# Kernel tuning notes

Hardware: AMD Instinct MI355X
Metric: run time of the kernel (lower is better)

The kernel has to match this reference:

```python
import jax, jax.numpy as jnp
import numpy as np

N = 6144; E = 98304; H = 256; HEADS = 4; NE = 8; TOPK = 2; S = 400; L = 3; V = 1024; T = 768
GAMMA = 2.0; LAMBDA_SPD = 0.5


def _ln(x, g, b):
    m = x.mean(-1, keepdims=True)
    v = ((x - m) ** 2).mean(-1, keepdims=True)
    return (x - m) / jnp.sqrt(v + 1e-5) * g + b


def _gelu(x):
    return jax.nn.gelu(x, approximate=False)


def _cos(a, b):
    # torch F.cosine_similarity with eps=1e-8
    na = jnp.maximum(jnp.linalg.norm(a, axis=-1), 1e-8)
    nb = jnp.maximum(jnp.linalg.norm(b, axis=-1), 1e-8)
    return (a * b).sum(-1) / (na * nb)


def setup_inputs():
    key = jax.random.key(0)
    ks = jax.random.split(key, 30)
    w = lambda k, s: jax.random.normal(k, s, dtype=jnp.float32) * 0.02
    z = lambda s: jnp.zeros(s, jnp.float32)
    o = lambda s: jnp.ones(s, jnp.float32)
    return dict(
        feat_v=jax.random.normal(ks[0], (N, V), dtype=jnp.float32),
        feat_t=jax.random.normal(ks[1], (N, T), dtype=jnp.float32),
        spd_matrix=jax.random.uniform(ks[2], (N, N), dtype=jnp.float32) * 8.0,
        proj_v_w=w(ks[3], (V, H)), proj_v_b=z((H,)),
        proj_t_w=w(ks[4], (T, H)), proj_t_b=z((H,)),
        mask_token=jax.random.normal(ks[5], (H,), dtype=jnp.float32),
        gate_w=w(ks[6], (H, NE)), gate_b=z((NE,)),
        moe_w1=w(ks[7], (NE, H, H)), moe_b1=z((NE, H)),
        moe_ln_g=o((NE, H)), moe_ln_b=z((NE, H)),
        moe_w2=w(ks[8], (NE, H, H)), moe_b2=z((NE, H)),
        gat_fc=w(ks[9], (L, H, HEADS * H)),
        gat_al=w(ks[10], (L, HEADS, H)), gat_ar=w(ks[11], (L, HEADS, H)),
        gat_bias=z((L, HEADS, H)),
        dec_v_w1=w(ks[12], (H, H)), dec_v_b1=z((H,)),
        dec_v_ln_g=o((H,)), dec_v_ln_b=z((H,)),
        dec_v_w2=w(ks[13], (H, V)), dec_v_b2=z((V,)),
        dec_t_w1=w(ks[14], (H, H)), dec_t_b1=z((H,)),
        dec_t_ln_g=o((H,)), dec_t_ln_b=z((H,)),
        dec_t_w2=w(ks[15], (H, T)), dec_t_b2=z((T,)),
        spd_w1=w(ks[16], (2 * H, H)), spd_b1=z((H,)),
        spd_ln_g=o((H,)), spd_ln_b=z((H,)),
        spd_w2=w(ks[17], (H, 1)), spd_b2=z((1,)),
        src=jax.random.randint(ks[18], (E,), 0, N, dtype=jnp.int32),
        dst=jax.random.randint(ks[19], (E,), 0, N, dtype=jnp.int32),
        mask_int=jax.random.randint(ks[20], (N,), 0, 10, dtype=jnp.int32),
        sample_idx=jnp.sort(jax.random.randint(ks[21], (S,), 0, N, dtype=jnp.int32)),
    )


def _forward(feat_v, feat_t, spd_matrix, proj_v_w, proj_v_b, proj_t_w, proj_t_b, mask_token,
             gate_w, gate_b, moe_w1, moe_b1, moe_ln_g, moe_ln_b, moe_w2, moe_b2,
             gat_fc, gat_al, gat_ar, gat_bias,
             dec_v_w1, dec_v_b1, dec_v_ln_g, dec_v_ln_b, dec_v_w2, dec_v_b2,
             dec_t_w1, dec_t_b1, dec_t_ln_g, dec_t_ln_b, dec_t_w2, dec_t_b2,
             spd_w1, spd_b1, spd_ln_g, spd_ln_b, spd_w2, spd_b2,
             src, dst, mask_int, sample_idx):
    # project each domain to hidden and average (stack(...).mean(0))
    x = ((feat_v @ proj_v_w + proj_v_b) + (feat_t @ proj_t_w + proj_t_b)) * 0.5  # [N,H]
    mask = mask_int == 0  # ~feat_drop_rate of nodes
    x = jnp.where(mask[:, None], mask_token[None, :], x)
    # --- MoE: softmax gate, top-2 routing, dense experts ---
    gate = jax.nn.softmax(x @ gate_w + gate_b, axis=-1)          # [N,NE]
    tw, ti = jax.lax.top_k(gate, TOPK)
    tw = tw / tw.sum(-1, keepdims=True)
    eh = _gelu(_ln(jnp.einsum('nh,ehk->nek', x, moe_w1) + moe_b1, moe_ln_g, moe_ln_b))
    eo = jnp.einsum('nek,ekj->nej', eh, moe_w2) + moe_b2         # [N,NE,H]
    sel = jnp.take_along_axis(eo, ti[:, :, None], axis=1)        # [N,TOPK,H]
    h = (sel * tw[:, :, None]).sum(axis=1)                       # [N,H]
    # --- GATConv layers (dgl semantics), mean over heads ---
    for l in range(L):
        z = (h @ gat_fc[l]).reshape(N, HEADS, H)                 # [N,heads,H]
        el = (z * gat_al[l]).sum(-1)                             # [N,heads]
        er = (z * gat_ar[l]).sum(-1)
        e = jax.nn.leaky_relu(el[src] + er[dst], negative_slope=0.2)  # [E,heads]
        m = jax.ops.segment_max(e, dst, num_segments=N)
        ex = jnp.exp(e - m[dst])
        den = jax.ops.segment_sum(ex, dst, num_segments=N)
        alpha = ex / jnp.where(den > 0, den, 1.0)[dst]
        out = jax.ops.segment_sum(alpha[:, :, None] * z[src], dst, num_segments=N)
        h = (out + gat_bias[l]).mean(axis=1)                     # [N,H]
    # --- focal cosine reconstruction loss over masked nodes ---
    maskf = mask.astype(h.dtype)
    nm = jnp.maximum(maskf.sum(), 1.0)
    rec = jnp.zeros((), h.dtype)
    for w1, b1, g, b, w2, b2, tgt in ((dec_v_w1, dec_v_b1, dec_v_ln_g, dec_v_ln_b, dec_v_w2, dec_v_b2, feat_v),
                                      (dec_t_w1, dec_t_b1, dec_t_ln_g, dec_t_ln_b, dec_t_w2, dec_t_b2, feat_t)):
        r = _gelu(_ln(h @ w1 + b1, g, b)) @ w2 + b2
        sim = _cos(r, tgt)
        rec = rec + (((1.0 - sim) ** GAMMA) * maskf).sum() / nm
    # --- SPD loss on S sampled nodes, pairwise MLP decode ---
    se = h[sample_idx]                                           # [S,H]
    li = se @ spd_w1[:H]                                         # cat([xi,xj]) @ W1 split
    lj = se @ spd_w1[H:]
    pre = li[:, None, :] + lj[None, :, :] + spd_b1               # [S,S,H]
    pred = (_gelu(_ln(pre, spd_ln_g, spd_ln_b)) @ spd_w2)[..., 0] + spd_b2[0]
    strue = spd_matrix[sample_idx][:, sample_idx]
    spd_loss = jnp.mean((pred - strue) ** 2)
    total = rec + LAMBDA_SPD * spd_loss
    return total, h


def reference(feat_v, feat_t, spd_matrix, proj_v_w, proj_v_b, proj_t_w, proj_t_b, mask_token,
              gate_w, gate_b, moe_w1, moe_b1, moe_ln_g, moe_ln_b, moe_w2, moe_b2,
              gat_fc, gat_al, gat_ar, gat_bias,
              dec_v_w1, dec_v_b1, dec_v_ln_g, dec_v_ln_b, dec_v_w2, dec_v_b2,
              dec_t_w1, dec_t_b1, dec_t_ln_g, dec_t_ln_b, dec_t_w2, dec_t_b2,
              spd_w1, spd_b1, spd_ln_g, spd_ln_b, spd_w2, spd_b2,
              src, dst, mask_int, sample_idx):
    return _forward(feat_v, feat_t, spd_matrix, proj_v_w, proj_v_b, proj_t_w, proj_t_b, mask_token,
                    gate_w, gate_b, moe_w1, moe_b1, moe_ln_g, moe_ln_b, moe_w2, moe_b2,
                    gat_fc, gat_al, gat_ar, gat_bias,
                    dec_v_w1, dec_v_b1, dec_v_ln_g, dec_v_ln_b, dec_v_w2, dec_v_b2,
                    dec_t_w1, dec_t_b1, dec_t_ln_g, dec_t_ln_b, dec_t_w2, dec_t_b2,
                    spd_w1, spd_b1, spd_ln_g, spd_ln_b, spd_w2, spd_b2,
                    src, dst, mask_int, sample_idx)
```

## Files before the change

### kernel.cpp

```cpp
#include <hip/hip_runtime.h>

#define NN 6144
#define EE 98304
#define HH 256
#define NHEADS 4
#define NEXP 8
#define SS 400
#define VV 1024
#define TT 768

__device__ __forceinline__ float wave_allsum(float v){
  #pragma unroll
  for (int off=32; off; off>>=1) v += __shfl_xor(v, off, 64);
  return v;
}
__device__ __forceinline__ float wave_allmax(float v){
  #pragma unroll
  for (int off=32; off; off>>=1) v = fmaxf(v, __shfl_xor(v, off, 64));
  return v;
}
__device__ __forceinline__ float block_allsum(float v, float* red){
  int t = threadIdx.x;
  v = wave_allsum(v);
  __syncthreads();
  if ((t & 63) == 0) red[t >> 6] = v;
  __syncthreads();
  return red[0] + red[1] + red[2] + red[3];
}
__device__ __forceinline__ float gelu_exact(float x){
  return 0.5f * x * (1.0f + erff(x * 0.70710678118654752f));
}
__device__ __forceinline__ float leaky02(float x){
  return x >= 0.f ? x : 0.2f * x;
}

template<bool ACC>
__global__ __launch_bounds__(256) void gemm_f32(const float* __restrict__ A,
    const float* __restrict__ B, float* __restrict__ C, int M, int Nc, int K){
  __shared__ float As[16][65];
  __shared__ float Bs[16][64];
  int t = threadIdx.x;
  int tx = t & 15, ty = t >> 4;
  int m0 = blockIdx.y * 64, n0 = blockIdx.x * 64;
  float acc[4][4] = {};
  for (int k0 = 0; k0 < K; k0 += 16){
    int ca = t & 15, ra = t >> 4;
    #pragma unroll
    for (int p = 0; p < 4; p++)
      As[ca][ra + p*16] = A[(size_t)(m0 + ra + p*16) * K + k0 + ca];
    int nb = t & 63, kb = t >> 6;
    #pragma unroll
    for (int p = 0; p < 4; p++)
      Bs[kb + p*4][nb] = B[(size_t)(k0 + kb + p*4) * Nc + n0 + nb];
    __syncthreads();
    #pragma unroll
    for (int kk = 0; kk < 16; kk++){
      float a[4], b[4];
      #pragma unroll
      for (int i = 0; i < 4; i++) a[i] = As[kk][ty*4 + i];
      #pragma unroll
      for (int j = 0; j < 4; j++) b[j] = Bs[kk][tx*4 + j];
      #pragma unroll
      for (int i = 0; i < 4; i++)
        #pragma unroll
        for (int j = 0; j < 4; j++) acc[i][j] += a[i] * b[j];
    }
    __syncthreads();
  }
  #pragma unroll
  for (int i = 0; i < 4; i++){
    int m = m0 + ty*4 + i;
    #pragma unroll
    for (int j = 0; j < 4; j++){
      int n = n0 + tx*4 + j;
      size_t idx = (size_t)m * Nc + n;
      C[idx] = (ACC ? C[idx] : 0.0f) + acc[i][j];
    }
  }
}

__global__ void xfin_kernel(const float* __restrict__ tmp, const float* __restrict__ pvb,
                            const float* __restrict__ ptb, const float* __restrict__ mtok,
                            const int* __restrict__ mask_int, float* __restrict__ x){
  int i = blockIdx.x * 256 + threadIdx.x;
  int n = i >> 8, j = i & 255;
  bool m = (mask_int[n] == 0);
  x[i] = m ? mtok[j] : 0.5f * (tmp[i] + pvb[j] + ptb[j]);
}

__global__ void mlist_kernel(const int* __restrict__ mask_int, int* mlist, int* mcount){
  int n = blockIdx.x * 256 + threadIdx.x;
  if (n < NN && mask_int[n] == 0){
    int p = atomicAdd(mcount, 1);
    mlist[p] = n;
  }
}

__global__ __launch_bounds__(256) void gate_topk_kernel(const float* __restrict__ x,
    const float* __restrict__ gw, const float* __restrict__ gb,
    int* __restrict__ ti, float* __restrict__ twt){
  int n = blockIdx.x, t = threadIdx.x;
  __shared__ float sx[256];
  __shared__ float logits[8];
  sx[t] = x[(size_t)n*256 + t];
  __syncthreads();
  int e = t >> 5, lane = t & 31;
  float p = 0.f;
  for (int h2 = lane; h2 < 256; h2 += 32) p += sx[h2] * gw[h2*8 + e];
  #pragma unroll
  for (int off = 16; off; off >>= 1) p += __shfl_down(p, off, 32);
  if (lane == 0) logits[e] = p + gb[e];
  __syncthreads();
  if (t == 0){
    float mx = -3.0e38f;
    #pragma unroll
    for (int i = 0; i < 8; i++) mx = fmaxf(mx, logits[i]);
    float g[8], s = 0.f;
    #pragma unroll
    for (int i = 0; i < 8; i++){ g[i] = expf(logits[i] - mx); s += g[i]; }
    #pragma unroll
    for (int i = 0; i < 8; i++) g[i] /= s;
    int i0 = 0;
    for (int i = 1; i < 8; i++) if (g[i] > g[i0]) i0 = i;
    int i1 = (i0 == 0) ? 1 : 0;
    for (int i = 0; i < 8; i++) if (i != i0 && g[i] > g[i1]) i1 = i;
    float w0 = g[i0], w1 = g[i1], sw = w0 + w1;
    ti[n*2] = i0; ti[n*2+1] = i1;
    twt[n*2] = w0 / sw; twt[n*2+1] = w1 / sw;
  }
}

__global__ __launch_bounds__(256) void moe_kernel(const float* __restrict__ x,
    const int* __restrict__ ti, const float* __restrict__ twt,
    const float* __restrict__ w1, const float* __restrict__ b1,
    const float* __restrict__ lng, const float* __restrict__ lnb,
    const float* __restrict__ w2, const float* __restrict__ b2,
    float* __restrict__ h){
  int n = blockIdx.x, t = threadIdx.x;
  __shared__ float sx[256], sh[256];
  __shared__ float red[4];
  sx[t] = x[(size_t)n*256 + t];
  float acc = 0.f;
  for (int k = 0; k < 2; k++){
    int e = ti[n*2 + k];
    float wgt = twt[n*2 + k];
    const float* W1 = w1 + (size_t)e * 65536;
    const float* W2 = w2 + (size_t)e * 65536;
    __syncthreads();
    float s = b1[e*256 + t];
    for (int hh = 0; hh < 256; hh++) s += sx[hh] * W1[hh*256 + t];
    float mean = block_allsum(s, red) * (1.f/256.f);
    float d = s - mean;
    float var = block_allsum(d*d, red) * (1.f/256.f);
    float nrm = d * rsqrtf(var + 1e-5f) * lng[e*256 + t] + lnb[e*256 + t];
    float ge = gelu_exact(nrm);
    __syncthreads();
    sh[t] = ge;
    __syncthreads();
    float o = b2[e*256 + t];
    for (int kk = 0; kk < 256; kk++) o += sh[kk] * W2[kk*256 + t];
    acc += wgt * o;
  }
  h[(size_t)n*256 + t] = acc;
}

__global__ void csr_count(const int* __restrict__ dst, int* counts){
  int e = blockIdx.x * 256 + threadIdx.x;
  if (e < EE) atomicAdd(&counts[dst[e]], 1);
}
__global__ __launch_bounds__(1024) void csr_scan(const int* __restrict__ counts, int* offs){
  __shared__ int part[1024];
  int t = threadIdx.x;
  int base = t * 6;
  int c[6]; int s = 0;
  #pragma unroll
  for (int q = 0; q < 6; q++){ c[q] = counts[base + q]; s += c[q]; }
  part[t] = s;
  __syncthreads();
  for (int off = 1; off < 1024; off <<= 1){
    int add = (t >= off) ? part[t - off] : 0;
    __syncthreads();
    part[t] += add;
    __syncthreads();
  }
  int excl = (t == 0) ? 0 : part[t-1];
  #pragma unroll
  for (int q = 0; q < 6; q++){ offs[base + q] = excl; excl += c[q]; }
  if (t == 1023) offs[NN] = excl;
}
__global__ void csr_fill(const int* __restrict__ src, const int* __restrict__ dst,
                         const int* __restrict__ offs, int* cursors, int* esrc){
  int e = blockIdx.x * 256 + threadIdx.x;
  if (e < EE){
    int d = dst[e];
    int pos = offs[d] + atomicAdd(&cursors[d], 1);
    esrc[pos] = src[e];
  }
}

__global__ __launch_bounds__(256) void eler_kernel(const float* __restrict__ z,
    const float* __restrict__ al, const float* __restrict__ ar,
    float* __restrict__ el, float* __restrict__ er){
  int n = blockIdx.x, t = threadIdx.x;
  int hd = t >> 6, lane = t & 63;
  const float* zr = z + (size_t)n*1024 + hd*256;
  float pl = 0.f, pr = 0.f;
  #pragma unroll
  for (int q = 0; q < 4; q++){
    int j = lane + q*64;
    float zv = zr[j];
    pl += zv * al[hd*256 + j];
    pr += zv * ar[hd*256 + j];
  }
  pl = wave_allsum(pl);
  pr = wave_allsum(pr);
  if (lane == 0){ el[n*4 + hd] = pl; er[n*4 + hd] = pr; }
}

__global__ __launch_bounds__(256) void gat_agg(const float* __restrict__ z,
    const float* __restrict__ el, const float* __restrict__ er,
    const int* __restrict__ offs, const int* __restrict__ esrc,
    const float* __restrict__ bias, float* __restrict__ hout){
  int n = blockIdx.x, t = threadIdx.x;
  int beg = offs[n], end = offs[n+1], deg = end - beg;
  __shared__ float ser[4];
  __shared__ float rbuf[4][4];
  __shared__ float smax[4], sden[4];
  __shared__ int ssrc[64];
  __shared__ float sal[64][4];
  if (t < 4) ser[t] = er[n*4 + t];
  __syncthreads();
  float acc4[4] = {0.f, 0.f, 0.f, 0.f};
  if (deg > 0){
    float mx[4] = {-3.0e38f, -3.0e38f, -3.0e38f, -3.0e38f};
    for (int i = t; i < deg; i += 256){
      int s = esrc[beg + i];
      #pragma unroll
      for (int hd = 0; hd < 4; hd++){
        float ev = leaky02(el[s*4 + hd] + ser[hd]);
        mx[hd] = fmaxf(mx[hd], ev);
      }
    }
    #pragma unroll
    for (int hd = 0; hd < 4; hd++) mx[hd] = wave_allmax(mx[hd]);
    if ((t & 63) == 0){
      #pragma unroll
      for (int hd = 0; hd < 4; hd++) rbuf[t >> 6][hd] = mx[hd];
    }
    __syncthreads();
    if (t < 4) smax[t] = fmaxf(fmaxf(rbuf[0][t], rbuf[1][t]), fmaxf(rbuf[2][t], rbuf[3][t]));
    __syncthreads();
    float sum_[4] = {0.f, 0.f, 0.f, 0.f};
    for (int i = t; i < deg; i += 256){
      int s = esrc[beg + i];
      #pragma unroll
      for (int hd = 0; hd < 4; hd++){
        float ev = leaky02(el[s*4 + hd] + ser[hd]);
        sum_[hd] += expf(ev - smax[hd]);
      }
    }
    #pragma unroll
    for (int hd = 0; hd < 4; hd++) sum_[hd] = wave_allsum(sum_[hd]);
    if ((t & 63) == 0){
      #pragma unroll
      for (int hd = 0; hd < 4; hd++) rbuf[t >> 6][hd] = sum_[hd];
    }
    __syncthreads();
    if (t < 4){
      float den = rbuf[0][t] + rbuf[1][t] + rbuf[2][t] + rbuf[3][t];
      sden[t] = (den > 0.f) ? 1.f / den : 1.f;
    }
    __syncthreads();
    for (int base = 0; base < deg; base += 64){
      int cnt = min(64, deg - base);
      __syncthreads();
      if (t < cnt){
        int s = esrc[beg + base + t];
        ssrc[t] = s;
        #pragma unroll
        for (int hd = 0; hd < 4; hd++){
          float ev = leaky02(el[s*4 + hd] + ser[hd]);
          sal[t][hd] = expf(ev - smax[hd]) * sden[hd];
        }
      }
      __syncthreads();
      for (int i = 0; i < cnt; i++){
        const float* zp = z + (size_t)ssrc[i] * 1024;
        #pragma unroll
        for (int hd = 0; hd < 4; hd++) acc4[hd] += sal[i][hd] * zp[hd*256 + t];
      }
    }
  }
  float o = 0.f;
  #pragma unroll
  for (int hd = 0; hd < 4; hd++) o += acc4[hd] + bias[hd*256 + t];
  hout[(size_t)n*256 + t] = 0.25f * o;
}

__global__ __launch_bounds__(256) void rec_kernel(const float* __restrict__ h,
    const int* __restrict__ mlist, const int* __restrict__ mcount,
    const float* __restrict__ w1, const float* __restrict__ b1,
    const float* __restrict__ g, const float* __restrict__ bb,
    const float* __restrict__ w2, const float* __restrict__ b2,
    const float* __restrict__ tgt, int Vd, float* __restrict__ acc_out){
  int idx = blockIdx.x;
  if (idx >= *mcount) return;
  int n = mlist[idx];
  int t = threadIdx.x;
  __shared__ float sx[256], sh[256];
  __shared__ float red[4];
  sx[t] = h[(size_t)n*256 + t];
  __syncthreads();
  float s = b1[t];
  for (int hh = 0; hh < 256; hh++) s += sx[hh] * w1[hh*256 + t];
  float mean = block_allsum(s, red) * (1.f/256.f);
  float d = s - mean;
  float var = block_allsum(d*d, red) * (1.f/256.f);
  float nrm = d * rsqrtf(var + 1e-5f) * g[t] + bb[t];
  float ge = gelu_exact(nrm);
  __syncthreads();
  sh[t] = ge;
  __syncthreads();
  float dot = 0.f, nr = 0.f, nt = 0.f;
  for (int j = t; j < Vd; j += 256){
    float r = b2[j];
    for (int k = 0; k < 256; k++) r += sh[k] * w2[(size_t)k*Vd + j];
    float tg = tgt[(size_t)n*Vd + j];
    dot += r * tg; nr += r * r; nt += tg * tg;
  }
  dot = block_allsum(dot, red);
  __syncthreads();
  nr = block_allsum(nr, red);
  __syncthreads();
  nt = block_allsum(nt, red);
  if (t == 0){
    float sim = dot / (fmaxf(sqrtf(nr), 1e-8f) * fmaxf(sqrtf(nt), 1e-8f));
    float f = 1.f - sim;
    atomicAdd(acc_out, f * f);
  }
}

__global__ __launch_bounds__(256) void spd_lin_kernel(const float* __restrict__ h,
    const int* __restrict__ sidx, const float* __restrict__ w1,
    float* __restrict__ li, float* __restrict__ lj){
  int i = blockIdx.x, t = threadIdx.x;
  __shared__ float sx[256];
  int n = sidx[i];
  sx[t] = h[(size_t)n*256 + t];
  __syncthreads();
  float a = 0.f, b = 0.f;
  for (int hh = 0; hh < 256; hh++){
    float xv = sx[hh];
    a += xv * w1[hh*256 + t];
    b += xv * w1[(256 + hh)*256 + t];
  }
  li[i*256 + t] = a;
  lj[i*256 + t] = b;
}

__global__ __launch_bounds__(256) void spd_pair_kernel(const float* __restrict__ li,
    const float* __restrict__ lj, const float* __restrict__ b1,
    const float* __restrict__ lng, const float* __restrict__ lnb,
    const float* __restrict__ w2, const float* __restrict__ b2,
    const float* __restrict__ spd, const int* __restrict__ sidx,
    float* __restrict__ buckets){
  int wid = threadIdx.x >> 6, lane = threadIdx.x & 63;
  int pair = blockIdx.x * 4 + wid;
  int i = pair / SS, j = pair % SS;
  __shared__ float bsum[4];
  float v[4];
  float tot = 0.f;
  #pragma unroll
  for (int q = 0; q < 4; q++){
    int c = lane + q*64;
    v[q] = li[i*256 + c] + lj[j*256 + c] + b1[c];
    tot += v[q];
  }
  tot = wave_allsum(tot);
  float mean = tot * (1.f/256.f);
  float var = 0.f;
  #pragma unroll
  for (int q = 0; q < 4; q++){ float d = v[q] - mean; var += d*d; }
  var = wave_allsum(var) * (1.f/256.f);
  float rstd = rsqrtf(var + 1e-5f);
  float dotp = 0.f;
  #pragma unroll
  for (int q = 0; q < 4; q++){
    int c = lane + q*64;
    float nrm = (v[q] - mean) * rstd * lng[c] + lnb[c];
    dotp += gelu_exact(nrm) * w2[c];
  }
  dotp = wave_allsum(dotp);
  float contrib = 0.f;
  if (lane == 0){
    float pred = dotp + b2[0];
    float st = spd[(size_t)sidx[i] * NN + sidx[j]];
    float diff = pred - st;
    contrib = diff * diff;
  }
  if (lane == 0) bsum[wid] = contrib;
  __syncthreads();
  if (threadIdx.x == 0){
    float s = bsum[0] + bsum[1] + bsum[2] + bsum[3];
    atomicAdd(&buckets[blockIdx.x & 255], s);
  }
}

__global__ __launch_bounds__(256) void finalize_kernel(const float* __restrict__ rec_acc,
    const float* __restrict__ buckets, const int* __restrict__ mcount,
    float* __restrict__ out){
  __shared__ float red[4];
  int t = threadIdx.x;
  float v = buckets[t];
  float spd_sum = block_allsum(v, red);
  if (t == 0){
    float nm = fmaxf((float)(*mcount), 1.0f);
    out[0] = rec_acc[0] / nm + 0.5f * (spd_sum / (float)(SS * SS));
  }
}

__global__ void copy_h_kernel(const float* __restrict__ h, float* __restrict__ out){
  int i = blockIdx.x * 256 + threadIdx.x;
  out[1 + i] = h[i];
}

extern "C" void kernel_launch(void* const* d_in, const int* in_sizes, int n_in,
                              void* d_out, int out_size, void* d_ws, size_t ws_size,
                              hipStream_t stream){
  const float* feat_v   = (const float*)d_in[0];
  const float* feat_t   = (const float*)d_in[1];
  const float* spd_mat  = (const float*)d_in[2];
  const float* proj_v_w = (const float*)d_in[3];
  const float* proj_v_b = (const float*)d_in[4];
  const float* proj_t_w = (const float*)d_in[5];
  const float* proj_t_b = (const float*)d_in[6];
  const float* mask_tok = (const float*)d_in[7];
  const float* gate_w   = (const float*)d_in[8];
  const float* gate_b   = (const float*)d_in[9];
  const float* moe_w1   = (const float*)d_in[10];
  const float* moe_b1   = (const float*)d_in[11];
  const float* moe_lng  = (const float*)d_in[12];
  const float* moe_lnb  = (const float*)d_in[13];
  const float* moe_w2   = (const float*)d_in[14];
  const float* moe_b2   = (const float*)d_in[15];
  const float* gat_fc   = (const float*)d_in[16];
  const float* gat_al   = (const float*)d_in[17];
  const float* gat_ar   = (const float*)d_in[18];
  const float* gat_bias = (const float*)d_in[19];
  const float* dv_w1 = (const float*)d_in[20];
  const float* dv_b1 = (const float*)d_in[21];
  const float* dv_g  = (const float*)d_in[22];
  const float* dv_b  = (const float*)d_in[23];
  const float* dv_w2 = (const float*)d_in[24];
  const float* dv_b2 = (const float*)d_in[25];
  const float* dt_w1 = (const float*)d_in[26];
  const float* dt_b1 = (const float*)d_in[27];
  const float* dt_g  = (const float*)d_in[28];
  const float* dt_b  = (const float*)d_in[29];
  const float* dt_w2 = (const float*)d_in[30];
  const float* dt_b2 = (const float*)d_in[31];
  const float* spd_w1 = (const float*)d_in[32];
  const float* spd_b1 = (const float*)d_in[33];
  const float* spd_g  = (const float*)d_in[34];
  const float* spd_bb = (const float*)d_in[35];
  const float* spd_w2 = (const float*)d_in[36];
  const float* spd_b2 = (const float*)d_in[37];
  const int* src      = (const int*)d_in[38];
  const int* dst      = (const int*)d_in[39];
  const int* mask_int = (const int*)d_in[40];
  const int* sidx     = (const int*)d_in[41];

  char* ws = (char*)d_ws;
  size_t off = 0;
  auto carve = [&](size_t bytes) -> char* {
    char* p = ws + off;
    off = (off + bytes + 255) & ~(size_t)255;
    return p;
  };
  int* counts  = (int*)carve(NN * 4);
  int* cursors = (int*)carve(NN * 4);
  int* offs    = (int*)carve((NN + 1) * 4);
  int* mlist   = (int*)carve(NN * 4);
  int* mcount  = (int*)carve(4);
  float* rec_acc = (float*)carve(4);
  float* buckets = (float*)carve(256 * 4);
  int* esrc    = (int*)carve(EE * 4);
  int* ti      = (int*)carve(NN * 2 * 4);
  size_t ctl_bytes = off;
  float* twt = (float*)carve(NN * 2 * 4);
  float* tmp = (float*)carve((size_t)NN * HH * 4);
  float* x   = (float*)carve((size_t)NN * HH * 4);
  float* hA  = (float*)carve((size_t)NN * HH * 4);
  float* hB  = (float*)carve((size_t)NN * HH * 4);
  float* z   = (float*)carve((size_t)NN * NHEADS * HH * 4);
  float* el  = (float*)carve((size_t)NN * NHEADS * 4);
  float* er  = (float*)carve((size_t)NN * NHEADS * 4);
  float* li  = (float*)carve((size_t)SS * HH * 4);
  float* lj  = (float*)carve((size_t)SS * HH * 4);
  (void)ws_size; (void)in_sizes; (void)n_in; (void)out_size;

  hipMemsetAsync(ws, 0, ctl_bytes, stream);

  gemm_f32<false><<<dim3(HH/64, NN/64), 256, 0, stream>>>(feat_v, proj_v_w, tmp, NN, HH, VV);
  gemm_f32<true ><<<dim3(HH/64, NN/64), 256, 0, stream>>>(feat_t, proj_t_w, tmp, NN, HH, TT);
  xfin_kernel<<<NN * HH / 256, 256, 0, stream>>>(tmp, proj_v_b, proj_t_b, mask_tok, mask_int, x);
  mlist_kernel<<<NN / 256, 256, 0, stream>>>(mask_int, mlist, mcount);

  gate_topk_kernel<<<NN, 256, 0, stream>>>(x, gate_w, gate_b, ti, twt);
  moe_kernel<<<NN, 256, 0, stream>>>(x, ti, twt, moe_w1, moe_b1, moe_lng, moe_lnb,
                                     moe_w2, moe_b2, hA);

  csr_count<<<EE / 256, 256, 0, stream>>>(dst, counts);
  csr_scan<<<1, 1024, 0, stream>>>(counts, offs);
  csr_fill<<<EE / 256, 256, 0, stream>>>(src, dst, offs, cursors, esrc);

  float* hin = hA; float* hout_ = hB;
  for (int l = 0; l < 3; l++){
    gemm_f32<false><<<dim3(NHEADS*HH/64, NN/64), 256, 0, stream>>>(
        hin, gat_fc + (size_t)l * HH * NHEADS * HH, z, NN, NHEADS*HH, HH);
    eler_kernel<<<NN, 256, 0, stream>>>(z, gat_al + (size_t)l * NHEADS * HH,
                                        gat_ar + (size_t)l * NHEADS * HH, el, er);
    gat_agg<<<NN, 256, 0, stream>>>(z, el, er, offs, esrc,
                                    gat_bias + (size_t)l * NHEADS * HH, hout_);
    float* sw = hin; hin = hout_; hout_ = sw;
  }

  rec_kernel<<<NN, 256, 0, stream>>>(hin, mlist, mcount, dv_w1, dv_b1, dv_g, dv_b,
                                     dv_w2, dv_b2, feat_v, VV, rec_acc);
  rec_kernel<<<NN, 256, 0, stream>>>(hin, mlist, mcount, dt_w1, dt_b1, dt_g, dt_b,
                                     dt_w2, dt_b2, feat_t, TT, rec_acc);

  spd_lin_kernel<<<SS, 256, 0, stream>>>(hin, sidx, spd_w1, li, lj);
  spd_pair_kernel<<<SS * SS / 4, 256, 0, stream>>>(li, lj, spd_b1, spd_g, spd_bb,
                                                   spd_w2, spd_b2, spd_mat, sidx, buckets);

  finalize_kernel<<<1, 256, 0, stream>>>(rec_acc, buckets, mcount, (float*)d_out);
  copy_h_kernel<<<NN * HH / 256, 256, 0, stream>>>(hin, (float*)d_out);
}
```

Measured before the change: 1.381 ms.

## Replace FP32 SIMT GEMMs with bf16 MFMA GEMMs using pre-transposed weights

Replaces the scalar FP32 tiled GEMM with a bf16 MFMA kernel (16x16x32) on 128x64 tiles. The A operand is converted to bf16 on the fly, and the weights are transposed and converted to bf16 by a new kernel each call. It targets the input projection and GAT fc GEMMs, which make up a large share of the FLOPs. In exchange it adds transpose launches and reduced precision, which may hurt accuracy.

```diff
diff --git a/kernel.cpp b/kernel.cpp
--- a/kernel.cpp
+++ b/kernel.cpp
@@ -9,6 +9,10 @@
 #define VV 1024
 #define TT 768
 
+typedef __bf16 bf16x8 __attribute__((ext_vector_type(8)));
+typedef float f32x4 __attribute__((ext_vector_type(4)));
+typedef unsigned short u16x8 __attribute__((ext_vector_type(8)));
+
 __device__ __forceinline__ float wave_allsum(float v){
   #pragma unroll
   for (int off=32; off; off>>=1) v += __shfl_xor(v, off, 64);
@@ -33,48 +37,83 @@
 __device__ __forceinline__ float leaky02(float x){
   return x >= 0.f ? x : 0.2f * x;
 }
+__device__ __forceinline__ unsigned short f2bf(float f){
+  unsigned int u = __float_as_uint(f);
+  unsigned int r = (u + 0x7FFFu + ((u >> 16) & 1u)) >> 16;
+  return (unsigned short)r;
+}
+
+__global__ __launch_bounds__(256) void transpose_w(const float* __restrict__ B,
+    unsigned short* __restrict__ BT, int K, int N){
+  __shared__ float tl[32][33];
+  int n0 = blockIdx.x * 32, k0 = blockIdx.y * 32;
+  int tx = threadIdx.x & 31, ty = threadIdx.x >> 5;
+  #pragma unroll
+  for (int q = 0; q < 4; q++){
+    int k = ty + q*8;
+    tl[k][tx] = B[(size_t)(k0 + k) * N + n0 + tx];
+  }
+  __syncthreads();
+  #pragma unroll
+  for (int q = 0; q < 4; q++){
+    int n = ty + q*8;
+    BT[(size_t)(n0 + n) * K + k0 + tx] = f2bf(tl[tx][n]);
+  }
+}
 
 template<bool ACC>
-__global__ __launch_bounds__(256) void gemm_f32(const float* __restrict__ A,
-    const float* __restrict__ B, float* __restrict__ C, int M, int Nc, int K){
-  __shared__ float As[16][65];
-  __shared__ float Bs[16][64];
+__global__ __launch_bounds__(256) void gemm_bf16(const float* __restrict__ A,
+    const unsigned short* __restrict__ BT, float* __restrict__ C,
+    int M, int Nc, int K){
+  __shared__ unsigned short As[128][40];
+  __shared__ unsigned short Bs[64][40];
   int t = threadIdx.x;
-  int tx = t & 15, ty = t >> 4;
-  int m0 = blockIdx.y * 64, n0 = blockIdx.x * 64;
-  float acc[4][4] = {};
-  for (int k0 = 0; k0 < K; k0 += 16){
-    int ca = t & 15, ra = t >> 4;
-    #pragma unroll
-    for (int p = 0; p < 4; p++)
-      As[ca][ra + p*16] = A[(size_t)(m0 + ra + p*16) * K + k0 + ca];
-    int nb = t & 63, kb = t >> 6;
-    #pragma unroll
-    for (int p = 0; p < 4; p++)
-      Bs[kb + p*4][nb] = B[(size_t)(k0 + kb + p*4) * Nc + n0 + nb];
-    __syncthreads();
-    #pragma unroll
-    for (int kk = 0; kk < 16; kk++){
-      float a[4], b[4];
-      #pragma unroll
-      for (int i = 0; i < 4; i++) a[i] = As[kk][ty*4 + i];
-      #pragma unroll
-      for (int j = 0; j < 4; j++) b[j] = Bs[kk][tx*4 + j];
-      #pragma unroll
-      for (int i = 0; i < 4; i++)
-        #pragma unroll
-        for (int j = 0; j < 4; j++) acc[i][j] += a[i] * b[j];
-    }
-    __syncthreads();
-  }
-  #pragma unroll
-  for (int i = 0; i < 4; i++){
-    int m = m0 + ty*4 + i;
-    #pragma unroll
-    for (int j = 0; j < 4; j++){
-      int n = n0 + tx*4 + j;
-      size_t idx = (size_t)m * Nc + n;
-      C[idx] = (ACC ? C[idx] : 0.0f) + acc[i][j];
+  int m0 = blockIdx.y * 128, n0 = blockIdx.x * 64;
+  int wave = t >> 6, lane = t & 63;
+  int fr = lane & 15, fs = lane >> 4;
+  f32x4 acc[2][4] = {};
+
+  int ra = t >> 2, sa = t & 3;
+  for (int k0 = 0; k0 < K; k0 += 32){
+    __syncthreads();
+    {
+      const float* p = &A[(size_t)(m0 + ra) * K + k0 + sa*8];
+      f32x4 u0 = *(const f32x4*)p;
+      f32x4 u1 = *(const f32x4*)(p + 4);
+      u16x8 w;
+      #pragma unroll
+      for (int i = 0; i < 4; i++){ w[i] = f2bf(u0[i]); w[4+i] = f2bf(u1[i]); }
+      *(u16x8*)&As[ra][sa*8] = w;
+      p = &A[(size_t)(m0 + 64 + ra) * K + k0 + sa*8];
+      u0 = *(const f32x4*)p;
+      u1 = *(const f32x4*)(p + 4);
+      #pragma unroll
+      for (int i = 0; i < 4; i++){ w[i] = f2bf(u0[i]); w[4+i] = f2bf(u1[i]); }
+      *(u16x8*)&As[64 + ra][sa*8] = w;
+    }
+    *(u16x8*)&Bs[ra][sa*8] = *(const u16x8*)&BT[(size_t)(n0 + ra) * K + k0 + sa*8];
+    __syncthreads();
+
+    bf16x8 a0 = *(const bf16x8*)&As[wave*32 + fr][fs*8];
+    bf16x8 a1 = *(const bf16x8*)&As[wave*32 + 16 + fr][fs*8];
+    #pragma unroll
+    for (int c = 0; c < 4; c++){
+      bf16x8 b = *(const bf16x8*)&Bs[c*16 + fr][fs*8];
+      acc[0][c] = __builtin_amdgcn_mfma_f32_16x16x32_bf16(a0, b, acc[0][c], 0, 0, 0);
+      acc[1][c] = __builtin_amdgcn_mfma_f32_16x16x32_bf16(a1, b, acc[1][c], 0, 0, 0);
+    }
+  }
+  #pragma unroll
+  for (int sub = 0; sub < 2; sub++){
+    #pragma unroll
+    for (int c = 0; c < 4; c++){
+      #pragma unroll
+      for (int i = 0; i < 4; i++){
+        int m = m0 + wave*32 + sub*16 + fs*4 + i;
+        int n = n0 + c*16 + fr;
+        size_t idx = (size_t)m * Nc + n;
+        C[idx] = (ACC ? C[idx] : 0.0f) + acc[sub][c][i];
+      }
     }
   }
 }
@@ -497,12 +536,21 @@
   float* er  = (float*)carve((size_t)NN * NHEADS * 4);
   float* li  = (float*)carve((size_t)SS * HH * 4);
   float* lj  = (float*)carve((size_t)SS * HH * 4);
+  unsigned short* projvBT = (unsigned short*)carve((size_t)HH * VV * 2);
+  unsigned short* projtBT = (unsigned short*)carve((size_t)HH * TT * 2);
+  unsigned short* gatBT   = (unsigned short*)carve((size_t)3 * NHEADS*HH * HH * 2);
   (void)ws_size; (void)in_sizes; (void)n_in; (void)out_size;
 
   hipMemsetAsync(ws, 0, ctl_bytes, stream);
 
-  gemm_f32<false><<<dim3(HH/64, NN/64), 256, 0, stream>>>(feat_v, proj_v_w, tmp, NN, HH, VV);
-  gemm_f32<true ><<<dim3(HH/64, NN/64), 256, 0, stream>>>(feat_t, proj_t_w, tmp, NN, HH, TT);
+  transpose_w<<<dim3(HH/32, VV/32), 256, 0, stream>>>(proj_v_w, projvBT, VV, HH);
+  transpose_w<<<dim3(HH/32, TT/32), 256, 0, stream>>>(proj_t_w, projtBT, TT, HH);
+  for (int l = 0; l < 3; l++)
+    transpose_w<<<dim3(NHEADS*HH/32, HH/32), 256, 0, stream>>>(
+        gat_fc + (size_t)l * HH * NHEADS * HH, gatBT + (size_t)l * NHEADS*HH * HH, HH, NHEADS*HH);
+
+  gemm_bf16<false><<<dim3(HH/64, NN/128), 256, 0, stream>>>(feat_v, projvBT, tmp, NN, HH, VV);
+  gemm_bf16<true ><<<dim3(HH/64, NN/128), 256, 0, stream>>>(feat_t, projtBT, tmp, NN, HH, TT);
   xfin_kernel<<<NN * HH / 256, 256, 0, stream>>>(tmp, proj_v_b, proj_t_b, mask_tok, mask_int, x);
   mlist_kernel<<<NN / 256, 256, 0, stream>>>(mask_int, mlist, mcount);
 
@@ -516,8 +564,8 @@
 
   float* hin = hA; float* hout_ = hB;
   for (int l = 0; l < 3; l++){
-    gemm_f32<false><<<dim3(NHEADS*HH/64, NN/64), 256, 0, stream>>>(
-        hin, gat_fc + (size_t)l * HH * NHEADS * HH, z, NN, NHEADS*HH, HH);
+    gemm_bf16<false><<<dim3(NHEADS*HH/64, NN/128), 256, 0, stream>>>(
+        hin, gatBT + (size_t)l * NHEADS*HH * HH, z, NN, NHEADS*HH, HH);
     eler_kernel<<<NN, 256, 0, stream>>>(z, gat_al + (size_t)l * NHEADS * HH,
                                         gat_ar + (size_t)l * NHEADS * HH, el, er);
     gat_agg<<<NN, 256, 0, stream>>>(z, el, er, offs, esrc,
```

Result: faster. 1.181 ms (-14.5%).
